# Performance work log

Measured on AMD Instinct MI355X. Metric: run time of the kernel, lower is better.

## Reference

```python
import jax, jax.numpy as jnp
import numpy as np

NUM_COMPONENTS = 4
HEADS = 16

def setup_inputs() -> dict:
    key = jax.random.key(0)
    ks = jax.random.split(key, 7)
    BC, S, D = 8, 4096, 1024   # batch*components, latent tokens, hidden dim
    E = 160                     # encoder (text) sequence length
    w_scale = 0.02              # keep logits in a sane range
    return {
        "hidden_states": jax.random.normal(ks[0], (BC, S, D), jnp.float32),
        "encoder_hidden_states": jax.random.normal(ks[1], (BC, E, D), jnp.float32),
        "Wq": jax.random.normal(ks[2], (D, D), jnp.float32) * w_scale,
        "Wk": jax.random.normal(ks[3], (D, D), jnp.float32) * w_scale,
        "Wv": jax.random.normal(ks[4], (D, D), jnp.float32) * w_scale,
        "Wo": jax.random.normal(ks[5], (D, D), jnp.float32) * w_scale,
        "bo": jnp.zeros((D,), jnp.float32),
    }

def reference(hidden_states, encoder_hidden_states, Wq, Wk, Wv, Wo, bo):
    BC, S, D = hidden_states.shape
    E = encoder_hidden_states.shape[1]
    C = NUM_COMPONENTS
    B = BC // C
    H = HEADS
    dh = D // H
    scale = dh ** -0.5

    # projections (diffusers to_q/to_k/to_v, no bias)
    q = hidden_states @ Wq            # [BC, S, D]
    k = encoder_hidden_states @ Wk    # [BC, E, D]
    v = encoder_hidden_states @ Wv    # [BC, E, D]

    q = q.reshape(BC, S, H, dh).transpose(0, 2, 1, 3)  # [BC, H, S, dh]
    k = k.reshape(BC, E, H, dh).transpose(0, 2, 1, 3)  # [BC, H, E, dh]
    v = v.reshape(BC, E, H, dh).transpose(0, 2, 1, 3)  # [BC, H, E, dh]

    scores = jnp.einsum("bhsd,bhtd->bhst", q, k) * scale  # [BC, H, S, E]
    scores_c = scores.reshape(C, B, H, S, E)

    # pooled (mean over encoder tokens) softmax across components
    pooled = scores_c.mean(axis=-1, keepdims=True)         # [C, B, H, S, 1]
    weights_pooled = jax.nn.softmax(pooled, axis=0)        # softmax over components
    # per-row softmax over encoder tokens, scaled by component weight
    weights = jax.nn.softmax(scores_c, axis=-1) * weights_pooled
    weights = weights.reshape(BC, H, S, E)

    out = jnp.einsum("bhst,bhtd->bhsd", weights, v)        # [BC, H, S, dh]
    out = out.transpose(0, 2, 1, 3).reshape(BC, S, D)

    out = out @ Wo + bo        # to_out[0]; to_out[1] is dropout (identity, eval)
    out = out + hidden_states  # residual_connection=True, rescale factor 1
    return out
```

## Files before the change

### kernel.cpp

```cpp
#include <hip/hip_runtime.h>
#include <stdint.h>

typedef __attribute__((ext_vector_type(8))) short short8;
typedef __attribute__((ext_vector_type(4))) float f32x4;
typedef __attribute__((ext_vector_type(4))) unsigned short us4;

#define DI __device__ __forceinline__

static constexpr int Dm = 1024;
static constexpr int Sm = 4096;
static constexpr int Em = 160;
static constexpr int Hm = 16;

static constexpr size_t OFF_HSB  = 0;
static constexpr size_t OFF_WT   = 67108864;
static constexpr size_t OFF_QB   = 75497472;
static constexpr size_t OFF_KB   = 142606336;
static constexpr size_t OFF_VT   = 147849216;
static constexpr size_t OFF_EHSB = 150994944;

DI unsigned short f2b(float f) {
  union { float f; unsigned u; } x; x.f = f;
  unsigned r = x.u + 0x7fffu + ((x.u >> 16) & 1u);
  return (unsigned short)(r >> 16);
}

DI void gl_lds16(const void* g, void* l) {
  __builtin_amdgcn_global_load_lds(
      (const __attribute__((address_space(1))) unsigned int*)g,
      (__attribute__((address_space(3))) unsigned int*)l, 16, 0, 0);
}

#define S_BARRIER __builtin_amdgcn_s_barrier()
#define LGKM0 do { asm volatile("s_waitcnt lgkmcnt(0)" ::: "memory"); __builtin_amdgcn_sched_barrier(0); } while (0)

__global__ void k_cvt(const float* __restrict__ in, unsigned short* __restrict__ out, int n4) {
  int stride = gridDim.x * blockDim.x;
  for (int i = blockIdx.x * blockDim.x + threadIdx.x; i < n4; i += stride) {
    float4 v = ((const float4*)in)[i];
    us4 o = { f2b(v.x), f2b(v.y), f2b(v.z), f2b(v.w) };
    *(us4*)(out + (size_t)i * 4) = o;
  }
}

__global__ void k_wtrans(const float* __restrict__ W0, const float* __restrict__ W1,
                         const float* __restrict__ W2, const float* __restrict__ W3,
                         unsigned short* __restrict__ Wt) {
  __shared__ float t[32][33];
  const float* W = (blockIdx.z == 0) ? W0 : (blockIdx.z == 1) ? W1 : (blockIdx.z == 2) ? W2 : W3;
  unsigned short* o = Wt + (size_t)blockIdx.z * 1048576;
  int tx = threadIdx.x, ty = threadIdx.y;
  int n = blockIdx.x * 32 + tx;
  int k0 = blockIdx.y * 32;
  #pragma unroll
  for (int j = ty; j < 32; j += 8) t[j][tx] = W[(size_t)(k0 + j) * 1024 + n];
  __syncthreads();
  #pragma unroll
  for (int j = ty; j < 32; j += 8)
    o[(size_t)(blockIdx.x * 32 + j) * 1024 + k0 + tx] = f2b(t[tx][j]);
}

template<int MODE>
__global__ __launch_bounds__(512, 2) void k_gemm256(const unsigned short* __restrict__ A,
                                                    const unsigned short* __restrict__ Bt,
                                                    void* __restrict__ Cout,
                                                    const float* __restrict__ bias,
                                                    const float* __restrict__ resid) {
  __shared__ __align__(16) char smem[131072];
  const int tid = threadIdx.x;
  const int lane = tid & 63;
  const int l15 = lane & 15;
  const int g = lane >> 4;
  const int wv = tid >> 6;
  const int wr = wv >> 2;
  const int wcn = wv & 3;
  const int bid = blockIdx.x;
  const int m0 = (((bid >> 5) << 3) + (bid & 7)) * 256;
  const int n0 = ((bid >> 3) & 3) * 256;

  f32x4 acc[8][4];
  #pragma unroll
  for (int i = 0; i < 8; ++i)
    #pragma unroll
    for (int j = 0; j < 4; ++j) acc[i][j] = (f32x4){0.f, 0.f, 0.f, 0.f};

  auto STG = [&](const unsigned short* G, int isB, int db, int hf, int tk) {
    int mn0 = isB ? n0 : m0;
    #pragma unroll
    for (int p = 0; p < 2; ++p) {
      int chl = p * 512 + tid;
      int rih = chl >> 3, j = chl & 7;
      int sj = (j ^ (rih & 7)) * 8;
      gl_lds16(G + (size_t)(mn0 + hf * 128 + rih) * 1024 + tk * 64 + sj,
               smem + isB * 65536 + db * 32768 + (hf * 1024 + chl) * 16);
    }
  };
  auto LDA = [&](short8 (&af)[2][4], int db, int mh) {
    const char* buf = smem + db * 32768;
    #pragma unroll
    for (int kk = 0; kk < 2; ++kk)
      #pragma unroll
      for (int mt = 0; mt < 4; ++mt)
        af[kk][mt] = *(const short8*)(buf + (wr * 128 + mh * 64 + mt * 16 + l15) * 128 +
                                      ((kk * 64 + g * 16) ^ ((l15 & 7) << 4)));
  };
  auto LDB = [&](short8 (&bf)[2][2], int db, int nh) {
    const char* buf = smem + 65536 + db * 32768;
    #pragma unroll
    for (int kk = 0; kk < 2; ++kk)
      #pragma unroll
      for (int nt = 0; nt < 2; ++nt)
        bf[kk][nt] = *(const short8*)(buf + (wcn * 64 + nh * 32 + nt * 16 + l15) * 128 +
                                      ((kk * 64 + g * 16) ^ ((l15 & 7) << 4)));
  };
  auto MM = [&](short8 (&af)[2][4], short8 (&bf)[2][2], int mh, int nh) {
    __builtin_amdgcn_s_setprio(1);
    #pragma unroll
    for (int kk = 0; kk < 2; ++kk)
      #pragma unroll
      for (int mt = 0; mt < 4; ++mt)
        #pragma unroll
        for (int nt = 0; nt < 2; ++nt)
          acc[mh * 4 + mt][nh * 2 + nt] = __builtin_amdgcn_mfma_f32_16x16x32_bf16(
              af[kk][mt], bf[kk][nt], acc[mh * 4 + mt][nh * 2 + nt], 0, 0, 0);
    __builtin_amdgcn_s_setprio(0);
    __builtin_amdgcn_sched_barrier(0);
  };

  STG(A, 0, 0, 0, 0); STG(Bt, 1, 0, 0, 0); STG(Bt, 1, 0, 1, 0); STG(A, 0, 0, 1, 0);
  STG(A, 0, 1, 0, 1); STG(Bt, 1, 1, 1, 1); STG(A, 0, 1, 1, 1);
  asm volatile("s_waitcnt vmcnt(6)" ::: "memory");
  S_BARRIER;

  short8 af[2][4], bf0[2][2], bf1[2][2];
  #pragma unroll 1
  for (int v = 0; v < 8; ++v) {
    const int t = 2 * v;
    const bool more = (v < 7);
    LDA(af, 0, 0); LDB(bf0, 0, 0);
    STG(Bt, 1, 1, 0, t + 1);
    S_BARRIER; LGKM0;
    MM(af, bf0, 0, 0);
    S_BARRIER;
    LDB(bf1, 0, 1);
    if (more) STG(A, 0, 0, 0, t + 2);
    S_BARRIER; LGKM0;
    MM(af, bf1, 0, 1);
    S_BARRIER;
    LDA(af, 0, 1);
    if (more) STG(Bt, 1, 0, 1, t + 2);
    S_BARRIER; LGKM0;
    MM(af, bf1, 1, 1);
    S_BARRIER;
    LDB(bf0, 0, 0);
    if (more) STG(A, 0, 0, 1, t + 2);
    S_BARRIER; LGKM0;
    MM(af, bf0, 1, 0);
    if (more) { asm volatile("s_waitcnt vmcnt(6)" ::: "memory"); }
    else      { asm volatile("s_waitcnt vmcnt(0)" ::: "memory"); }
    S_BARRIER;
    LDA(af, 1, 0); LDB(bf0, 1, 0);
    if (more) STG(Bt, 1, 0, 0, t + 2);
    S_BARRIER; LGKM0;
    MM(af, bf0, 0, 0);
    S_BARRIER;
    LDB(bf1, 1, 1);
    if (more) STG(A, 0, 1, 0, t + 3);
    S_BARRIER; LGKM0;
    MM(af, bf1, 0, 1);
    S_BARRIER;
    LDA(af, 1, 1);
    if (more) STG(Bt, 1, 1, 1, t + 3);
    S_BARRIER; LGKM0;
    MM(af, bf1, 1, 1);
    S_BARRIER;
    LDB(bf0, 1, 0);
    if (more) STG(A, 0, 1, 1, t + 3);
    S_BARRIER; LGKM0;
    MM(af, bf0, 1, 0);
    asm volatile("s_waitcnt vmcnt(6)" ::: "memory");
    S_BARRIER;
  }

  __syncthreads();
  if (MODE == 0) {
    unsigned short* Cl = (unsigned short*)smem;
    #pragma unroll
    for (int m = 0; m < 8; ++m)
      #pragma unroll
      for (int n = 0; n < 4; ++n)
        #pragma unroll
        for (int r = 0; r < 4; ++r)
          Cl[(wr * 128 + m * 16 + 4 * g + r) * 256 + wcn * 64 + n * 16 + l15] = f2b(acc[m][n][r]);
    __syncthreads();
    #pragma unroll
    for (int j = 0; j < 16; ++j) {
      int ch = j * 512 + tid;
      int row = ch >> 5, sl = ch & 31;
      *(short8*)((unsigned short*)Cout + (size_t)(m0 + row) * 1024 + n0 + sl * 8) =
          *(const short8*)(Cl + row * 256 + sl * 8);
    }
  } else {
    #pragma unroll
    for (int m = 0; m < 8; ++m)
      #pragma unroll
      for (int n = 0; n < 4; ++n)
        #pragma unroll
        for (int r = 0; r < 4; ++r) {
          size_t row = (size_t)(m0 + wr * 128 + m * 16 + 4 * g + r);
          int col = n0 + wcn * 64 + n * 16 + l15;
          size_t idx = row * 1024 + col;
          ((float*)Cout)[idx] = acc[m][n][r] + bias[col] + resid[idx];
        }
  }
}

__global__ __launch_bounds__(256, 2) void k_gemm_kv(const unsigned short* __restrict__ A,
                                                    const unsigned short* __restrict__ Wt,
                                                    unsigned short* __restrict__ kb,
                                                    unsigned short* __restrict__ vt) {
  __shared__ __align__(16) char smem[32768];
  char* As = smem;
  char* Bs = smem + 16384;
  const int tid = threadIdx.x;
  const int lane = tid & 63;
  const int l15 = lane & 15;
  const int g = lane >> 4;
  const int wv = tid >> 6;
  const int wr = wv >> 1, wc = wv & 1;
  const int m0 = blockIdx.x * 128, n0 = blockIdx.y * 128;
  const int z = blockIdx.z;
  const unsigned short* Bt = Wt + (size_t)(1 + z) * 1048576;

  f32x4 acc[4][4];
  #pragma unroll
  for (int i = 0; i < 4; ++i)
    #pragma unroll
    for (int j = 0; j < 4; ++j) acc[i][j] = (f32x4){0.f, 0.f, 0.f, 0.f};

  for (int t = 0; t < 16; ++t) {
    __syncthreads();
    #pragma unroll
    for (int is = 0; is < 4; ++is) {
      int ch = is * 256 + tid;
      int row = ch >> 3, j = ch & 7;
      int sj = (j ^ (row & 7)) * 8;
      gl_lds16(A  + (size_t)(m0 + row) * 1024 + t * 64 + sj, As + ch * 16);
      gl_lds16(Bt + (size_t)(n0 + row) * 1024 + t * 64 + sj, Bs + ch * 16);
    }
    __syncthreads();
    short8 af[2][4], bf[2][4];
    #pragma unroll
    for (int kk = 0; kk < 2; ++kk)
      #pragma unroll
      for (int mt = 0; mt < 4; ++mt) {
        af[kk][mt] = *(const short8*)(As + (wr * 64 + mt * 16 + l15) * 128 + ((kk * 64 + g * 16) ^ ((l15 & 7) << 4)));
        bf[kk][mt] = *(const short8*)(Bs + (wc * 64 + mt * 16 + l15) * 128 + ((kk * 64 + g * 16) ^ ((l15 & 7) << 4)));
      }
    #pragma unroll
    for (int kk = 0; kk < 2; ++kk)
      #pragma unroll
      for (int mt = 0; mt < 4; ++mt)
        #pragma unroll
        for (int nt = 0; nt < 4; ++nt)
          acc[mt][nt] = __builtin_amdgcn_mfma_f32_16x16x32_bf16(af[kk][mt], bf[kk][nt], acc[mt][nt], 0, 0, 0);
  }

  #pragma unroll
  for (int mt = 0; mt < 4; ++mt)
    #pragma unroll
    for (int nt = 0; nt < 4; ++nt)
      #pragma unroll
      for (int r = 0; r < 4; ++r) {
        int row = m0 + wr * 64 + mt * 16 + 4 * g + r;
        int col = n0 + wc * 64 + nt * 16 + l15;
        unsigned short hv = f2b(acc[mt][nt][r]);
        if (z == 0) {
          kb[(size_t)row * 1024 + col] = hv;
        } else {
          int bc = row / 160, e = row - bc * 160;
          vt[((size_t)(bc * 16 + (col >> 6)) * 64 + (col & 63)) * 192 + e] = hv;
        }
      }
}

__global__ __launch_bounds__(256, 2) void k_attn(const unsigned short* __restrict__ Qb,
                                                 const unsigned short* __restrict__ Kb,
                                                 const unsigned short* __restrict__ Vt,
                                                 unsigned short* __restrict__ AOb) {
  __shared__ __align__(16) char smem[22528];
  float* pooled = (float*)(smem + 21504);
  const int tid = threadIdx.x, lane = tid & 63, wv = tid >> 6;
  const int g = lane >> 4, l15 = lane & 15;
  const int s0 = blockIdx.x * 64;
  const int h = blockIdx.y;
  const int b = blockIdx.z;
  const int bc = wv * 2 + b;
  const float scale = 0.125f;

  const unsigned short* Qp = Qb + ((size_t)bc * Sm + s0) * Dm + h * 64;
  const unsigned short* Kp = Kb + (size_t)bc * Em * Dm + h * 64;
  const unsigned short* Vp = Vt + ((size_t)bc * Hm + h) * (64 * 192);
  unsigned short* Op = AOb + ((size_t)bc * Sm + s0) * Dm + h * 64;
  char* Pw = smem + wv * 5376;

  #pragma unroll 1
  for (int st = 0; st < 4; ++st) {
    short8 qf[2];
    #pragma unroll
    for (int kk = 0; kk < 2; ++kk)
      qf[kk] = *(const short8*)(Qp + (size_t)(st * 16 + l15) * Dm + kk * 32 + g * 8);
    f32x4 sc[10];
    #pragma unroll
    for (int et = 0; et < 10; ++et) {
      sc[et] = (f32x4){0.f, 0.f, 0.f, 0.f};
      #pragma unroll
      for (int kk = 0; kk < 2; ++kk) {
        short8 kf = *(const short8*)(Kp + (size_t)(et * 16 + l15) * Dm + kk * 32 + g * 8);
        sc[et] = __builtin_amdgcn_mfma_f32_16x16x32_bf16(qf[kk], kf, sc[et], 0, 0, 0);
      }
    }
    float rs4[4];
    #pragma unroll
    for (int r = 0; r < 4; ++r) {
      float v = 0.f;
      #pragma unroll
      for (int et = 0; et < 10; ++et) v += sc[et][r];
      v += __shfl_xor(v, 1); v += __shfl_xor(v, 2); v += __shfl_xor(v, 4); v += __shfl_xor(v, 8);
      if (l15 == 0) pooled[(st * 16 + 4 * g + r) * 4 + wv] = v * (scale / 160.f);
      float mx = sc[0][r];
      #pragma unroll
      for (int et = 1; et < 10; ++et) mx = fmaxf(mx, sc[et][r]);
      mx = fmaxf(mx, __shfl_xor(mx, 1)); mx = fmaxf(mx, __shfl_xor(mx, 2));
      mx = fmaxf(mx, __shfl_xor(mx, 4)); mx = fmaxf(mx, __shfl_xor(mx, 8));
      float rs = 0.f;
      #pragma unroll
      for (int et = 0; et < 10; ++et) {
        float p = __expf((sc[et][r] - mx) * scale);
        rs += p;
        *(unsigned short*)(Pw + (4 * g + r) * 336 + (et * 16 + l15) * 2) = f2b(p);
      }
      rs += __shfl_xor(rs, 1); rs += __shfl_xor(rs, 2); rs += __shfl_xor(rs, 4); rs += __shfl_xor(rs, 8);
      rs4[r] = rs;
    }
    f32x4 oa[4];
    #pragma unroll
    for (int dt = 0; dt < 4; ++dt) oa[dt] = (f32x4){0.f, 0.f, 0.f, 0.f};
    #pragma unroll
    for (int k5 = 0; k5 < 5; ++k5) {
      short8 pf = *(const short8*)(Pw + l15 * 336 + k5 * 64 + g * 16);
      #pragma unroll
      for (int dt = 0; dt < 4; ++dt) {
        short8 vf = *(const short8*)(Vp + (size_t)(dt * 16 + l15) * 192 + k5 * 32 + g * 8);
        oa[dt] = __builtin_amdgcn_mfma_f32_16x16x32_bf16(pf, vf, oa[dt], 0, 0, 0);
      }
    }
    __syncthreads();
    #pragma unroll
    for (int r = 0; r < 4; ++r) {
      float4 pl = *(const float4*)&pooled[(st * 16 + 4 * g + r) * 4];
      float m3 = fmaxf(fmaxf(pl.x, pl.y), fmaxf(pl.z, pl.w));
      float ssum = __expf(pl.x - m3) + __expf(pl.y - m3) + __expf(pl.z - m3) + __expf(pl.w - m3);
      float mine = (wv == 0) ? pl.x : (wv == 1) ? pl.y : (wv == 2) ? pl.z : pl.w;
      float srw = __expf(mine - m3) / (ssum * rs4[r]);
      #pragma unroll
      for (int dt = 0; dt < 4; ++dt)
        Op[(size_t)(st * 16 + 4 * g + r) * Dm + dt * 16 + l15] = f2b(oa[dt][r] * srw);
    }
  }
}

extern "C" void kernel_launch(void* const* d_in, const int* in_sizes, int n_in,
                              void* d_out, int out_size, void* d_ws, size_t ws_size,
                              hipStream_t stream) {
  const float* hs  = (const float*)d_in[0];
  const float* ehs = (const float*)d_in[1];
  const float* Wq  = (const float*)d_in[2];
  const float* Wk  = (const float*)d_in[3];
  const float* Wv  = (const float*)d_in[4];
  const float* Wo  = (const float*)d_in[5];
  const float* bo  = (const float*)d_in[6];
  char* ws = (char*)d_ws;
  unsigned short* hsb = (unsigned short*)(ws + OFF_HSB);
  unsigned short* wt  = (unsigned short*)(ws + OFF_WT);
  unsigned short* qb  = (unsigned short*)(ws + OFF_QB);
  unsigned short* kb  = (unsigned short*)(ws + OFF_KB);
  unsigned short* vt  = (unsigned short*)(ws + OFF_VT);
  unsigned short* eb  = (unsigned short*)(ws + OFF_EHSB);

  hipLaunchKernelGGL(k_cvt, dim3(1280), dim3(256), 0, stream, ehs, eb, 8 * 160 * 1024 / 4);
  hipLaunchKernelGGL(k_wtrans, dim3(32, 32, 4), dim3(32, 8), 0, stream, Wq, Wk, Wv, Wo, wt);
  hipLaunchKernelGGL(k_gemm_kv, dim3(10, 8, 2), dim3(256), 0, stream, eb, wt, kb, vt);
  hipLaunchKernelGGL(k_cvt, dim3(2048), dim3(256), 0, stream, hs, hsb, 8 * 4096 * 1024 / 4);
  hipLaunchKernelGGL((k_gemm256<0>), dim3(512), dim3(512), 0, stream, hsb, wt, (void*)qb,
                     (const float*)nullptr, (const float*)nullptr);
  hipLaunchKernelGGL(k_attn, dim3(64, 16, 2), dim3(256), 0, stream, qb, kb, vt, hsb);
  hipLaunchKernelGGL((k_gemm256<1>), dim3(512), dim3(512), 0, stream, hsb, wt + 3 * 1048576, d_out, bo, hs);
}
```

Before: 349.8 us.

## Reschedule GEMM LDS pipeline to reuse B fragments and use inline ds_read_b128

Reworks the double-buffered GEMM main loop so the fourth MFMA sub-step reuses the bf0 fragment loaded earlier instead of reloading it from LDS. The global-to-LDS staging order and the vmcnt wait thresholds are changed to match. LDS reads are now emitted as inline-asm ds_read_b128 with precomputed base and swizzle offsets, which cuts address arithmetic. This removes one LDS read phase and one lgkm wait per half-iteration. The tighter ordering of buffer overwrites and waits could introduce races if it is wrong.

```diff
diff --git a/kernel.cpp b/kernel.cpp
--- a/kernel.cpp
+++ b/kernel.cpp
@@ -31,8 +31,15 @@
       (__attribute__((address_space(3))) unsigned int*)l, 16, 0, 0);
 }
 
+DI short8 lds_rd128(unsigned off) {
+  float4 d;
+  asm volatile("ds_read_b128 %0, %1" : "=&v"(d) : "v"(off));
+  union { float4 f; short8 s; } u; u.f = d; return u.s;
+}
+
 #define S_BARRIER __builtin_amdgcn_s_barrier()
 #define LGKM0 do { asm volatile("s_waitcnt lgkmcnt(0)" ::: "memory"); __builtin_amdgcn_sched_barrier(0); } while (0)
+#define VMCNT(n) asm volatile("s_waitcnt vmcnt(" #n ")" ::: "memory")
 
 __global__ void k_cvt(const float* __restrict__ in, unsigned short* __restrict__ out, int n4) {
   int stride = gridDim.x * blockDim.x;
@@ -78,6 +85,14 @@
   const int m0 = (((bid >> 5) << 3) + (bid & 7)) * 256;
   const int n0 = ((bid >> 3) & 3) * 256;
 
+  typedef __attribute__((address_space(3))) char c3;
+  const unsigned lds0 = (unsigned)(size_t)(c3*)smem;
+  unsigned swz[2];
+  swz[0] = (unsigned)((g * 16) ^ ((l15 & 7) << 4));
+  swz[1] = (unsigned)((64 + g * 16) ^ ((l15 & 7) << 4));
+  const unsigned baseA = lds0 + (unsigned)((wr * 128 + l15) * 128);
+  const unsigned baseB = lds0 + 65536u + (unsigned)((wcn * 64 + l15) * 128);
+
   f32x4 acc[8][4];
   #pragma unroll
   for (int i = 0; i < 8; ++i)
@@ -96,22 +111,18 @@
     }
   };
   auto LDA = [&](short8 (&af)[2][4], int db, int mh) {
-    const char* buf = smem + db * 32768;
     #pragma unroll
     for (int kk = 0; kk < 2; ++kk)
       #pragma unroll
       for (int mt = 0; mt < 4; ++mt)
-        af[kk][mt] = *(const short8*)(buf + (wr * 128 + mh * 64 + mt * 16 + l15) * 128 +
-                                      ((kk * 64 + g * 16) ^ ((l15 & 7) << 4)));
+        af[kk][mt] = lds_rd128(baseA + (unsigned)(db * 32768 + mh * 8192 + mt * 2048) + swz[kk]);
   };
   auto LDB = [&](short8 (&bf)[2][2], int db, int nh) {
-    const char* buf = smem + 65536 + db * 32768;
     #pragma unroll
     for (int kk = 0; kk < 2; ++kk)
       #pragma unroll
       for (int nt = 0; nt < 2; ++nt)
-        bf[kk][nt] = *(const short8*)(buf + (wcn * 64 + nh * 32 + nt * 16 + l15) * 128 +
-                                      ((kk * 64 + g * 16) ^ ((l15 & 7) << 4)));
+        bf[kk][nt] = lds_rd128(baseB + (unsigned)(db * 32768 + nh * 4096 + nt * 2048) + swz[kk]);
   };
   auto MM = [&](short8 (&af)[2][4], short8 (&bf)[2][2], int mh, int nh) {
     __builtin_amdgcn_s_setprio(1);
@@ -127,9 +138,9 @@
     __builtin_amdgcn_sched_barrier(0);
   };
 
-  STG(A, 0, 0, 0, 0); STG(Bt, 1, 0, 0, 0); STG(Bt, 1, 0, 1, 0); STG(A, 0, 0, 1, 0);
-  STG(A, 0, 1, 0, 1); STG(Bt, 1, 1, 1, 1); STG(A, 0, 1, 1, 1);
-  asm volatile("s_waitcnt vmcnt(6)" ::: "memory");
+  STG(A, 0, 0, 0, 0); STG(A, 0, 0, 1, 0); STG(Bt, 1, 0, 0, 0); STG(Bt, 1, 0, 1, 0);
+  STG(Bt, 1, 1, 0, 1); STG(Bt, 1, 1, 1, 1);
+  VMCNT(4);
   S_BARRIER;
 
   short8 af[2][4], bf0[2][2], bf1[2][2];
@@ -138,47 +149,44 @@
     const int t = 2 * v;
     const bool more = (v < 7);
     LDA(af, 0, 0); LDB(bf0, 0, 0);
-    STG(Bt, 1, 1, 0, t + 1);
+    STG(A, 0, 1, 0, t + 1);
     S_BARRIER; LGKM0;
     MM(af, bf0, 0, 0);
     S_BARRIER;
     LDB(bf1, 0, 1);
+    STG(A, 0, 1, 1, t + 1);
+    S_BARRIER; LGKM0;
+    MM(af, bf1, 0, 1);
+    S_BARRIER;
+    LDA(af, 0, 1);
+    if (more) STG(Bt, 1, 0, 0, t + 2);
+    S_BARRIER; LGKM0;
+    MM(af, bf1, 1, 1);
+    S_BARRIER;
+    if (more) STG(Bt, 1, 0, 1, t + 2);
+    S_BARRIER;
+    MM(af, bf0, 1, 0);
+    if (more) { VMCNT(4); } else { VMCNT(0); }
+    S_BARRIER;
+    LDA(af, 1, 0); LDB(bf0, 1, 0);
     if (more) STG(A, 0, 0, 0, t + 2);
     S_BARRIER; LGKM0;
+    MM(af, bf0, 0, 0);
+    S_BARRIER;
+    LDB(bf1, 1, 1);
+    if (more) STG(A, 0, 0, 1, t + 2);
+    S_BARRIER; LGKM0;
     MM(af, bf1, 0, 1);
     S_BARRIER;
-    LDA(af, 0, 1);
-    if (more) STG(Bt, 1, 0, 1, t + 2);
+    LDA(af, 1, 1);
+    if (more) STG(Bt, 1, 1, 0, t + 3);
     S_BARRIER; LGKM0;
     MM(af, bf1, 1, 1);
     S_BARRIER;
-    LDB(bf0, 0, 0);
-    if (more) STG(A, 0, 0, 1, t + 2);
-    S_BARRIER; LGKM0;
+    if (more) STG(Bt, 1, 1, 1, t + 3);
+    S_BARRIER;
     MM(af, bf0, 1, 0);
-    if (more) { asm volatile("s_waitcnt vmcnt(6)" ::: "memory"); }
-    else      { asm volatile("s_waitcnt vmcnt(0)" ::: "memory"); }
-    S_BARRIER;
-    LDA(af, 1, 0); LDB(bf0, 1, 0);
-    if (more) STG(Bt, 1, 0, 0, t + 2);
-    S_BARRIER; LGKM0;
-    MM(af, bf0, 0, 0);
-    S_BARRIER;
-    LDB(bf1, 1, 1);
-    if (more) STG(A, 0, 1, 0, t + 3);
-    S_BARRIER; LGKM0;
-    MM(af, bf1, 0, 1);
-    S_BARRIER;
-    LDA(af, 1, 1);
-    if (more) STG(Bt, 1, 1, 1, t + 3);
-    S_BARRIER; LGKM0;
-    MM(af, bf1, 1, 1);
-    S_BARRIER;
-    LDB(bf0, 1, 0);
-    if (more) STG(A, 0, 1, 1, t + 3);
-    S_BARRIER; LGKM0;
-    MM(af, bf0, 1, 0);
-    asm volatile("s_waitcnt vmcnt(6)" ::: "memory");
+    VMCNT(4);
     S_BARRIER;
   }
 
```

After: 503.4 us. 43.9% more time.
